# Performance work log

Measured on AMD Instinct MI355X. Metric: run time of the kernel, lower is better.

Reference implementation:

```python
import jax, jax.numpy as jnp
import numpy as np
from jax import lax


def _conv(x, w, padding, groups=1):
    # NCHW / OIHW 2D conv, stride 1
    return lax.conv_general_dilated(
        x, w, window_strides=(1, 1), padding=padding,
        dimension_numbers=("NCHW", "OIHW", "NCHW"),
        feature_group_count=groups)


def setup_inputs() -> dict:
    key = jax.random.key(0)
    ks = jax.random.split(key, 5)
    B, C, H, W = 8, 192, 128, 128
    HEADS = 8
    rgb = jax.random.normal(ks[0], (B, C, H, W), dtype=jnp.float32)
    ir = jax.random.normal(ks[1], (B, C, H, W), dtype=jnp.float32)
    w_qkv = jax.random.normal(ks[2], (3 * C, C, 1, 1), dtype=jnp.float32) * 0.02
    w_dw = jax.random.normal(ks[3], (3 * C, 1, 3, 3), dtype=jnp.float32) * 0.02
    w_proj = jax.random.normal(ks[4], (C, C, 1, 1), dtype=jnp.float32) * 0.02
    temperature = jnp.ones((HEADS, 1, 1), dtype=jnp.float32)
    return {"rgb": rgb, "ir": ir, "w_qkv": w_qkv, "w_dw": w_dw,
            "w_proj": w_proj, "temperature": temperature}


def reference(rgb, ir, w_qkv, w_dw, w_proj, temperature):
    heads = temperature.shape[0]
    b, c, h, w = rgb.shape
    hd = c // heads  # per-head channel count

    def qkv(x):
        y = _conv(x, w_qkv, "VALID")                 # [b, 3c, h, w]
        y = _conv(y, w_dw, "SAME", groups=3 * c)      # depthwise 3x3
        q, k, v = jnp.split(y, 3, axis=1)
        rs = lambda t: t.reshape(b, heads, hd, h * w)  # b head c (h w)
        return rs(q), rs(k), rs(v)

    rq, rk, rv = qkv(rgb)
    iq, ik, iv = qkv(ir)

    # torch F.normalize(dim=-1): x / max(||x||_2, 1e-12)
    nrm = lambda t: t / jnp.maximum(jnp.linalg.norm(t, axis=-1, keepdims=True), 1e-12)
    rq, rk, iq, ik = nrm(rq), nrm(rk), nrm(iq), nrm(ik)

    # channel-wise (transposed) cross attention: [b,h,hd,hd] attn matrices
    attn_ir = jax.nn.softmax(jnp.einsum("bhcn,bhdn->bhcd", rq, ik) * temperature, axis=-1)
    attn_rgb = jax.nn.softmax(jnp.einsum("bhcn,bhdn->bhcd", iq, rk) * temperature, axis=-1)

    out_ir = jnp.einsum("bhcd,bhdn->bhcn", attn_ir, iv).reshape(b, c, h, w)
    out_rgb = jnp.einsum("bhcd,bhdn->bhcn", attn_rgb, rv).reshape(b, c, h, w)

    out_ir = _conv(out_ir, w_proj, "VALID")
    out_rgb = _conv(out_rgb, w_proj, "VALID")
    return out_rgb, out_ir
```

## Files before the change

### kernel.cpp

```cpp
#include <hip/hip_runtime.h>

#define N_PIX 16384
#define CC    192
#define C3    576
#define KK    192
#define HD    24

typedef __attribute__((ext_vector_type(8))) short short8;
typedef __attribute__((ext_vector_type(4))) float f32x4;

__device__ __forceinline__ unsigned short f2bf(float x) {
    unsigned u = __float_as_uint(x);
    u += 0x7fff + ((u >> 16) & 1);
    return (unsigned short)(u >> 16);
}
__device__ __forceinline__ float bf2f(unsigned short s) {
    return __uint_as_float(((unsigned)s) << 16);
}
__device__ __forceinline__ int pack2(unsigned short lo, unsigned short hi) {
    return (int)(((unsigned)hi << 16) | (unsigned)lo);
}

__global__ __launch_bounds__(256) void cvt_f32_bf16(const float* __restrict__ src,
                                                    unsigned short* __restrict__ dst, int n4) {
    int i = blockIdx.x * 256 + threadIdx.x;
    if (i < n4) {
        float4 v = ((const float4*)src)[i];
        ushort4 o;
        o.x = f2bf(v.x); o.y = f2bf(v.y); o.z = f2bf(v.z); o.w = f2bf(v.w);
        ((ushort4*)dst)[i] = o;
    }
}

template<bool B_F32, bool C_BF16>
__device__ __forceinline__ void mfma_gemm(const unsigned short* __restrict__ Abf,
                                          const void* __restrict__ Bsrc,
                                          void* __restrict__ Cdst,
                                          int m0, int n0) {
    __shared__ unsigned short As[192][44];
    __shared__ unsigned short Bs[128][44];

    const int tid  = threadIdx.x;
    const int wave = tid >> 6, lane = tid & 63;
    const int quad = lane >> 4, l15 = lane & 15;
    const int wr = wave >> 2, wc = wave & 3;

    f32x4 acc[6][2];
#pragma unroll
    for (int i = 0; i < 6; i++)
#pragma unroll
        for (int j = 0; j < 2; j++) acc[i][j] = (f32x4)0.f;

    const int kg = tid & 7;
    const int n2 = tid >> 3;

    for (int k0 = 0; k0 < KK; k0 += 32) {
        {
            int row = tid >> 2, kc = (tid & 3) * 8;
            *(int4*)&As[row][kc] = *(const int4*)(Abf + (long)(m0 + row) * KK + k0 + kc);
            if (tid < 256) {
                int ch = tid + 512;
                int row2 = ch >> 2, kc2 = (ch & 3) * 8;
                *(int4*)&As[row2][kc2] = *(const int4*)(Abf + (long)(m0 + row2) * KK + k0 + kc2);
            }
        }
        if (B_F32) {
            const float* Bp = (const float*)Bsrc;
            float2 v[4];
#pragma unroll
            for (int j = 0; j < 4; j++)
                v[j] = *(const float2*)(Bp + (long)(k0 + kg * 4 + j) * N_PIX + n0 + n2 * 2);
#pragma unroll
            for (int i = 0; i < 2; i++) {
                unsigned short us[4];
#pragma unroll
                for (int j = 0; j < 4; j++) us[j] = f2bf(i ? v[j].y : v[j].x);
                int2 pk = make_int2(pack2(us[0], us[1]), pack2(us[2], us[3]));
                *(int2*)&Bs[n2 * 2 + i][kg * 4] = pk;
            }
        } else {
            const unsigned short* Bp = (const unsigned short*)Bsrc;
            ushort2 v[4];
#pragma unroll
            for (int j = 0; j < 4; j++)
                v[j] = *(const ushort2*)(Bp + (long)(k0 + kg * 4 + j) * N_PIX + n0 + n2 * 2);
#pragma unroll
            for (int i = 0; i < 2; i++) {
                unsigned short us[4];
#pragma unroll
                for (int j = 0; j < 4; j++) us[j] = i ? v[j].y : v[j].x;
                int2 pk = make_int2(pack2(us[0], us[1]), pack2(us[2], us[3]));
                *(int2*)&Bs[n2 * 2 + i][kg * 4] = pk;
            }
        }
        __syncthreads();

        short8 a[6], b[2];
#pragma unroll
        for (int mi = 0; mi < 6; mi++)
            a[mi] = *(const short8*)&As[wr * 96 + mi * 16 + l15][quad * 8];
#pragma unroll
        for (int ni = 0; ni < 2; ni++)
            b[ni] = *(const short8*)&Bs[wc * 32 + ni * 16 + l15][quad * 8];
#pragma unroll
        for (int mi = 0; mi < 6; mi++)
#pragma unroll
            for (int ni = 0; ni < 2; ni++)
                acc[mi][ni] = __builtin_amdgcn_mfma_f32_16x16x32_bf16(a[mi], b[ni], acc[mi][ni], 0, 0, 0);
        __syncthreads();
    }

#pragma unroll
    for (int mi = 0; mi < 6; mi++)
#pragma unroll
        for (int ni = 0; ni < 2; ni++)
#pragma unroll
            for (int r = 0; r < 4; r++) {
                int row = m0 + wr * 96 + mi * 16 + quad * 4 + r;
                int col = n0 + wc * 32 + ni * 16 + l15;
                if (C_BF16)
                    ((unsigned short*)Cdst)[(long)row * N_PIX + col] = f2bf(acc[mi][ni][r]);
                else
                    ((float*)Cdst)[(long)row * N_PIX + col] = acc[mi][ni][r];
            }
}

__global__ __launch_bounds__(512, 4) void qkv_mfma(const unsigned short* __restrict__ wbf,
                                                   const float* __restrict__ rgb,
                                                   const float* __restrict__ ir,
                                                   unsigned short* __restrict__ Ybf) {
    const int z = blockIdx.z, mod = z >> 3, b = z & 7;
    const float* x = (mod ? ir : rgb) + (long)b * CC * N_PIX;
    unsigned short* y = Ybf + (long)z * C3 * N_PIX;
    mfma_gemm<true, true>(wbf, x, y, blockIdx.y * 192, blockIdx.x * 128);
}

__global__ __launch_bounds__(512, 4) void out_mfma(const unsigned short* __restrict__ weff,
                                                   const unsigned short* __restrict__ Zbf,
                                                   float* __restrict__ out) {
    const int z = blockIdx.z;
    const unsigned short* V = Zbf + ((long)z * C3 + 2 * CC) * N_PIX;
    float* C = out + (long)z * CC * N_PIX;
    mfma_gemm<false, false>(weff + (long)z * CC * CC, V, C, 0, blockIdx.x * 128);
}

__global__ __launch_bounds__(256) void dwconv3x3(const unsigned short* __restrict__ Ybf,
                                                 const float* __restrict__ wdw,
                                                 unsigned short* __restrict__ Zbf) {
    const int z  = blockIdx.z;
    const int oc = blockIdx.y;
    const int idx = blockIdx.x * 256 + threadIdx.x;
    const int p0  = idx * 8;
    const int h   = p0 >> 7;
    const int w0  = p0 & 127;
    const int wq  = threadIdx.x & 15;
    const unsigned short* Yc = Ybf + ((long)z * C3 + oc) * N_PIX;

    float wk[9];
#pragma unroll
    for (int i = 0; i < 9; i++) wk[i] = wdw[oc * 9 + i];

    float f[3][8];
#pragma unroll
    for (int ry = 0; ry < 3; ry++) {
        const int hy = h + ry - 1;
        int4 raw = make_int4(0, 0, 0, 0);
        if (hy >= 0 && hy <= 127)
            raw = *(const int4*)(Yc + hy * 128 + w0);
        f[ry][0] = bf2f((unsigned short)(raw.x & 0xffff));
        f[ry][1] = bf2f((unsigned short)((unsigned)raw.x >> 16));
        f[ry][2] = bf2f((unsigned short)(raw.y & 0xffff));
        f[ry][3] = bf2f((unsigned short)((unsigned)raw.y >> 16));
        f[ry][4] = bf2f((unsigned short)(raw.z & 0xffff));
        f[ry][5] = bf2f((unsigned short)((unsigned)raw.z >> 16));
        f[ry][6] = bf2f((unsigned short)(raw.w & 0xffff));
        f[ry][7] = bf2f((unsigned short)((unsigned)raw.w >> 16));
    }

    float acc[8];
#pragma unroll
    for (int j = 0; j < 8; j++) acc[j] = 0.f;

#pragma unroll
    for (int ry = 0; ry < 3; ry++) {
        float l = __shfl_up(f[ry][7], 1);
        float r = __shfl_down(f[ry][0], 1);
        if (wq == 0)  l = 0.f;
        if (wq == 15) r = 0.f;
        const float wl = wk[ry * 3 + 0], wc = wk[ry * 3 + 1], wr = wk[ry * 3 + 2];
        acc[0] = fmaf(wl, l, acc[0]);
#pragma unroll
        for (int j = 1; j < 8; j++) acc[j] = fmaf(wl, f[ry][j - 1], acc[j]);
#pragma unroll
        for (int j = 0; j < 8; j++) acc[j] = fmaf(wc, f[ry][j], acc[j]);
#pragma unroll
        for (int j = 0; j < 7; j++) acc[j] = fmaf(wr, f[ry][j + 1], acc[j]);
        acc[7] = fmaf(wr, r, acc[7]);
    }

    ushort4 o[2];
    unsigned short* po = (unsigned short*)o;
#pragma unroll
    for (int j = 0; j < 8; j++) po[j] = f2bf(acc[j]);
    *(int4*)(Zbf + ((long)z * C3 + oc) * N_PIX + p0) = *(const int4*)o;
}

__global__ __launch_bounds__(64) void gram_partial(const unsigned short* __restrict__ Zbf,
                                                   float* __restrict__ gpart) {
    const int split = blockIdx.x;
    const int bh    = blockIdx.y;
    const int which = blockIdx.z;
    const int b = bh >> 3, head = bh & 7;
    const int zq = (which == 0) ? b : 8 + b;
    const int zk = (which == 0) ? 8 + b : b;
    const unsigned short* Q  = Zbf + ((long)zq * C3 + head * HD) * N_PIX;
    const unsigned short* Kr = Zbf + ((long)zk * C3 + CC + head * HD) * N_PIX;

    __shared__ float Qc[24][132];
    __shared__ float Kc[24][132];

    const int t = threadIdx.x;
    const int ci = t >> 3, di = t & 7;
    const int c0 = ci * 3, d0 = di * 3;

    float acc[3][3];
#pragma unroll
    for (int i = 0; i < 3; i++)
#pragma unroll
        for (int j = 0; j < 3; j++) acc[i][j] = 0.f;
    float ss = 0.f;

    const int n0base = split * 2048;
    for (int nc = 0; nc < 2048; nc += 128) {
        const long n0 = n0base + nc;
        const unsigned short* src = nullptr;
        float* dstrow = nullptr;
        if (t < 24)               { src = Q  + (long)t * N_PIX + n0;        dstrow = Qc[t]; }
        else if (t >= 32 && t < 56) { src = Kr + (long)(t - 32) * N_PIX + n0; dstrow = Kc[t - 32]; }
        if (src) {
#pragma unroll 4
            for (int i = 0; i < 16; i++) {
                int4 raw = *(const int4*)(src + i * 8);
                float f[8];
                f[0] = bf2f((unsigned short)(raw.x & 0xffff)); f[1] = bf2f((unsigned short)((unsigned)raw.x >> 16));
                f[2] = bf2f((unsigned short)(raw.y & 0xffff)); f[3] = bf2f((unsigned short)((unsigned)raw.y >> 16));
                f[4] = bf2f((unsigned short)(raw.z & 0xffff)); f[5] = bf2f((unsigned short)((unsigned)raw.z >> 16));
                f[6] = bf2f((unsigned short)(raw.w & 0xffff)); f[7] = bf2f((unsigned short)((unsigned)raw.w >> 16));
                *(float4*)&dstrow[i * 8]     = make_float4(f[0], f[1], f[2], f[3]);
                *(float4*)&dstrow[i * 8 + 4] = make_float4(f[4], f[5], f[6], f[7]);
#pragma unroll
                for (int q = 0; q < 8; q++) ss = fmaf(f[q], f[q], ss);
            }
        }
        __syncthreads();
#pragma unroll 4
        for (int kk = 0; kk < 128; kk += 4) {
            float4 qv[3], kv[3];
#pragma unroll
            for (int i = 0; i < 3; i++) qv[i] = *(const float4*)&Qc[c0 + i][kk];
#pragma unroll
            for (int j = 0; j < 3; j++) kv[j] = *(const float4*)&Kc[d0 + j][kk];
#pragma unroll
            for (int i = 0; i < 3; i++)
#pragma unroll
                for (int j = 0; j < 3; j++)
                    acc[i][j] += qv[i].x * kv[j].x + qv[i].y * kv[j].y +
                                 qv[i].z * kv[j].z + qv[i].w * kv[j].w;
        }
        __syncthreads();
    }

    const int g = (which * 64 + bh) * 8 + split;
    float* gp = gpart + (long)g * 624;
#pragma unroll
    for (int i = 0; i < 3; i++)
#pragma unroll
        for (int j = 0; j < 3; j++)
            gp[(c0 + i) * 24 + (d0 + j)] = acc[i][j];
    if (t < 24) gp[576 + t] = ss;
    else if (t >= 32 && t < 56) gp[600 + (t - 32)] = ss;
}

__global__ __launch_bounds__(256) void gram_reduce_softmax(const float* __restrict__ gpart,
                                                           const float* __restrict__ temperature,
                                                           float* __restrict__ P) {
    const int g = blockIdx.x;
    const int head = g & 7;
    __shared__ float Gs[576];
    __shared__ float qs[24], ks[24], invq[24], invk[24];

    const int t = threadIdx.x;
    for (int e = t; e < 624; e += 256) {
        float s = 0.f;
        for (int sp = 0; sp < 8; sp++) s += gpart[(long)(g * 8 + sp) * 624 + e];
        if (e < 576) Gs[e] = s;
        else if (e < 600) qs[e - 576] = s;
        else ks[e - 600] = s;
    }
    __syncthreads();
    if (t < 24) {
        invq[t] = 1.f / fmaxf(sqrtf(qs[t]), 1e-12f);
        invk[t] = 1.f / fmaxf(sqrtf(ks[t]), 1e-12f);
    }
    __syncthreads();
    if (t < 24) {
        const float temp = temperature[head];
        float row[24];
        float m = -1e30f;
#pragma unroll
        for (int d = 0; d < 24; d++) {
            row[d] = Gs[t * 24 + d] * invq[t] * invk[d] * temp;
            m = fmaxf(m, row[d]);
        }
        float ssum = 0.f;
#pragma unroll
        for (int d = 0; d < 24; d++) {
            row[d] = expf(row[d] - m);
            ssum += row[d];
        }
        const float inv = 1.f / ssum;
#pragma unroll
        for (int d = 0; d < 24; d++)
            P[(long)g * 576 + t * 24 + d] = row[d] * inv;
    }
}

__global__ __launch_bounds__(256) void build_weff(const float* __restrict__ wproj,
                                                  const float* __restrict__ P,
                                                  unsigned short* __restrict__ weff) {
    const int o = blockIdx.z, b = blockIdx.y;
    const int e = blockIdx.x * 256 + threadIdx.x;
    const int co = e / 192, col = e % 192;
    const int head = col / 24, d = col % 24;
    const int which = 1 - o;
    const float* Pp = P + (long)(which * 64 + b * 8 + head) * 576;
    const float* wp = wproj + co * 192 + head * 24;
    float acc = 0.f;
#pragma unroll
    for (int hc = 0; hc < 24; hc++)
        acc = fmaf(wp[hc], Pp[hc * 24 + d], acc);
    weff[((long)(o * 8 + b) * 192 + co) * 192 + col] = f2bf(acc);
}

extern "C" void kernel_launch(void* const* d_in, const int* in_sizes, int n_in,
                              void* d_out, int out_size, void* d_ws, size_t ws_size,
                              hipStream_t stream) {
    (void)in_sizes; (void)n_in; (void)out_size; (void)ws_size;
    const float* rgb    = (const float*)d_in[0];
    const float* ir     = (const float*)d_in[1];
    const float* w_qkv  = (const float*)d_in[2];
    const float* w_dw   = (const float*)d_in[3];
    const float* w_proj = (const float*)d_in[4];
    const float* temp   = (const float*)d_in[5];
    float* out = (float*)d_out;

    char* wsb = (char*)d_ws;
    unsigned short* Y_bf    = (unsigned short*)(wsb);
    unsigned short* Z_bf    = (unsigned short*)(wsb + 301989888L);
    unsigned short* w_bf    = (unsigned short*)(wsb + 603979776L);
    unsigned short* weff_bf = (unsigned short*)(wsb + 604200960L);
    float*          gpart   = (float*)(wsb + 605380608L);
    float*          P       = (float*)(wsb + 607936512L);

    cvt_f32_bf16<<<108, 256, 0, stream>>>(w_qkv, w_bf, 27648);
    qkv_mfma<<<dim3(128, 3, 16), 512, 0, stream>>>(w_bf, rgb, ir, Y_bf);
    dwconv3x3<<<dim3(8, 576, 16), 256, 0, stream>>>(Y_bf, w_dw, Z_bf);
    gram_partial<<<dim3(8, 64, 2), 64, 0, stream>>>(Z_bf, gpart);
    gram_reduce_softmax<<<128, 256, 0, stream>>>(gpart, temp, P);
    build_weff<<<dim3(144, 8, 2), 256, 0, stream>>>(w_proj, P, weff_bf);
    out_mfma<<<dim3(128, 1, 16), 512, 0, stream>>>(weff_bf, Z_bf, out);
}
```

Before: 807.5 us.

## Pre-transpose inputs to bf16 and pipeline QKV GEMM with direct global-to-LDS loads

Adds a kernel that converts the fp32 rgb/ir inputs to bf16 and transposes them to pixel-major layout, so the QKV GEMM can stream contiguous K-rows. The QKV GEMM is rewritten to use global_load_lds 16-byte transfers into XOR-swizzled, double-buffered shared memory with a K-step of 64. This removes per-thread fp32 to bf16 conversion and strided loads from the GEMM's inner loop. The cost is an extra pass over the inputs, and the Z buffer is reused as scratch for the transposed data.

```diff
diff --git a/kernel.cpp b/kernel.cpp
--- a/kernel.cpp
+++ b/kernel.cpp
@@ -5,6 +5,7 @@
 #define C3    576
 #define KK    192
 #define HD    24
+#define KS    64
 
 typedef __attribute__((ext_vector_type(8))) short short8;
 typedef __attribute__((ext_vector_type(4))) float f32x4;
@@ -19,6 +20,12 @@
 }
 __device__ __forceinline__ int pack2(unsigned short lo, unsigned short hi) {
     return (int)(((unsigned)hi << 16) | (unsigned)lo);
+}
+
+__device__ __forceinline__ void g2l16(const unsigned short* g, unsigned short* l) {
+    __builtin_amdgcn_global_load_lds(
+        (const __attribute__((address_space(1))) void*)g,
+        (__attribute__((address_space(3))) void*)l, 16, 0, 0);
 }
 
 __global__ __launch_bounds__(256) void cvt_f32_bf16(const float* __restrict__ src,
@@ -32,11 +39,126 @@
     }
 }
 
-template<bool B_F32, bool C_BF16>
-__device__ __forceinline__ void mfma_gemm(const unsigned short* __restrict__ Abf,
-                                          const void* __restrict__ Bsrc,
-                                          void* __restrict__ Cdst,
-                                          int m0, int n0) {
+__global__ __launch_bounds__(256) void cvtT(const float* __restrict__ rgb,
+                                            const float* __restrict__ ir,
+                                            unsigned short* __restrict__ xT) {
+    const int z  = blockIdx.y;
+    const int n0 = blockIdx.x * 128;
+    const float* x = ((z >= 8) ? ir : rgb) + (long)(z & 7) * CC * N_PIX;
+    __shared__ unsigned short T[192][136];
+
+    const int t = threadIdx.x;
+#pragma unroll
+    for (int i = 0; i < 24; i++) {
+        int q = i * 256 + t;
+        int k = q >> 5, nc = q & 31;
+        float4 v = *(const float4*)(x + (long)k * N_PIX + n0 + nc * 4);
+        ushort4 o;
+        o.x = f2bf(v.x); o.y = f2bf(v.y); o.z = f2bf(v.z); o.w = f2bf(v.w);
+        *(ushort4*)&T[k][nc * 4] = o;
+    }
+    __syncthreads();
+    unsigned short* dst = xT + ((long)z * N_PIX + n0) * CC;
+#pragma unroll
+    for (int i = 0; i < 12; i++) {
+        int c = i * 256 + t;
+        int n = c / 24, kc = c - n * 24;
+        unsigned short us[8];
+#pragma unroll
+        for (int j = 0; j < 8; j++) us[j] = T[kc * 8 + j][n];
+        int4 pk = make_int4(pack2(us[0], us[1]), pack2(us[2], us[3]),
+                            pack2(us[4], us[5]), pack2(us[6], us[7]));
+        *(int4*)(dst + (long)n * CC + kc * 8) = pk;
+    }
+}
+
+__global__ __launch_bounds__(512, 4) void qkv_mfma(const unsigned short* __restrict__ wbf,
+                                                   const unsigned short* __restrict__ xT,
+                                                   unsigned short* __restrict__ Ybf) {
+    const int z  = blockIdx.z;
+    const unsigned short* Bg = xT + (long)z * N_PIX * CC;
+    unsigned short* y = Ybf + (long)z * C3 * N_PIX;
+    const int m0 = blockIdx.y * 192, n0 = blockIdx.x * 128;
+
+    __shared__ unsigned short As[2][192 * 64];
+    __shared__ unsigned short Bs[2][128 * 64];
+
+    const int tid  = threadIdx.x;
+    const int wave = tid >> 6, lane = tid & 63;
+    const int quad = lane >> 4, l15 = lane & 15;
+    const int wr = wave >> 2, wc = wave & 3;
+
+    f32x4 acc[6][2];
+#pragma unroll
+    for (int i = 0; i < 6; i++)
+#pragma unroll
+        for (int j = 0; j < 2; j++) acc[i][j] = (f32x4)0.f;
+
+    auto stage = [&](int buf, int k0) {
+#pragma unroll
+        for (int s = 0; s < 3; s++) {
+            int j = s * 8 + wave;
+            int q = j * 64 + lane;
+            int m = q >> 3, c = (q & 7) ^ (m & 7);
+            g2l16(wbf + (long)(m0 + m) * KK + k0 + c * 8, &As[buf][j * 512]);
+        }
+#pragma unroll
+        for (int s = 0; s < 2; s++) {
+            int j = s * 8 + wave;
+            int q = j * 64 + lane;
+            int n = q >> 3, c = (q & 7) ^ (n & 7);
+            g2l16(Bg + (long)(n0 + n) * CC + k0 + c * 8, &Bs[buf][j * 512]);
+        }
+    };
+
+    stage(0, 0);
+    __syncthreads();
+    int cur = 0;
+    for (int it = 0; it < 3; ++it) {
+        if (it < 2) stage(cur ^ 1, (it + 1) * KS);
+        const unsigned short* A  = As[cur];
+        const unsigned short* Bl = Bs[cur];
+#pragma unroll
+        for (int kk = 0; kk < 2; kk++) {
+            short8 a[6], b[2];
+#pragma unroll
+            for (int mi = 0; mi < 6; mi++) {
+                int r = wr * 96 + mi * 16 + l15;
+                int c = (kk * 4 + quad) ^ (r & 7);
+                a[mi] = *(const short8*)&A[r * 64 + c * 8];
+            }
+#pragma unroll
+            for (int ni = 0; ni < 2; ni++) {
+                int n = wc * 32 + ni * 16 + l15;
+                int c = (kk * 4 + quad) ^ (n & 7);
+                b[ni] = *(const short8*)&Bl[n * 64 + c * 8];
+            }
+#pragma unroll
+            for (int mi = 0; mi < 6; mi++)
+#pragma unroll
+                for (int ni = 0; ni < 2; ni++)
+                    acc[mi][ni] = __builtin_amdgcn_mfma_f32_16x16x32_bf16(a[mi], b[ni], acc[mi][ni], 0, 0, 0);
+        }
+        __syncthreads();
+        cur ^= 1;
+    }
+
+#pragma unroll
+    for (int mi = 0; mi < 6; mi++)
+#pragma unroll
+        for (int ni = 0; ni < 2; ni++)
+#pragma unroll
+            for (int r = 0; r < 4; r++) {
+                int row = m0 + wr * 96 + mi * 16 + quad * 4 + r;
+                int col = n0 + wc * 32 + ni * 16 + l15;
+                y[(long)row * N_PIX + col] = f2bf(acc[mi][ni][r]);
+            }
+}
+
+__device__ __forceinline__ void mfma_gemm_old(const unsigned short* __restrict__ Abf,
+                                              const unsigned short* __restrict__ Bsrc,
+                                              float* __restrict__ Cdst,
+                                              int m0, int n0) {
     __shared__ unsigned short As[192][44];
     __shared__ unsigned short Bs[128][44];
 
@@ -64,26 +186,11 @@
                 *(int4*)&As[row2][kc2] = *(const int4*)(Abf + (long)(m0 + row2) * KK + k0 + kc2);
             }
         }
-        if (B_F32) {
-            const float* Bp = (const float*)Bsrc;
-            float2 v[4];
+        {
+            ushort2 v[4];
 #pragma unroll
             for (int j = 0; j < 4; j++)
-                v[j] = *(const float2*)(Bp + (long)(k0 + kg * 4 + j) * N_PIX + n0 + n2 * 2);
-#pragma unroll
-            for (int i = 0; i < 2; i++) {
-                unsigned short us[4];
-#pragma unroll
-                for (int j = 0; j < 4; j++) us[j] = f2bf(i ? v[j].y : v[j].x);
-                int2 pk = make_int2(pack2(us[0], us[1]), pack2(us[2], us[3]));
-                *(int2*)&Bs[n2 * 2 + i][kg * 4] = pk;
-            }
-        } else {
-            const unsigned short* Bp = (const unsigned short*)Bsrc;
-            ushort2 v[4];
-#pragma unroll
-            for (int j = 0; j < 4; j++)
-                v[j] = *(const ushort2*)(Bp + (long)(k0 + kg * 4 + j) * N_PIX + n0 + n2 * 2);
+                v[j] = *(const ushort2*)(Bsrc + (long)(k0 + kg * 4 + j) * N_PIX + n0 + n2 * 2);
 #pragma unroll
             for (int i = 0; i < 2; i++) {
                 unsigned short us[4];
@@ -118,21 +225,8 @@
             for (int r = 0; r < 4; r++) {
                 int row = m0 + wr * 96 + mi * 16 + quad * 4 + r;
                 int col = n0 + wc * 32 + ni * 16 + l15;
-                if (C_BF16)
-                    ((unsigned short*)Cdst)[(long)row * N_PIX + col] = f2bf(acc[mi][ni][r]);
-                else
-                    ((float*)Cdst)[(long)row * N_PIX + col] = acc[mi][ni][r];
-            }
-}
-
-__global__ __launch_bounds__(512, 4) void qkv_mfma(const unsigned short* __restrict__ wbf,
-                                                   const float* __restrict__ rgb,
-                                                   const float* __restrict__ ir,
-                                                   unsigned short* __restrict__ Ybf) {
-    const int z = blockIdx.z, mod = z >> 3, b = z & 7;
-    const float* x = (mod ? ir : rgb) + (long)b * CC * N_PIX;
-    unsigned short* y = Ybf + (long)z * C3 * N_PIX;
-    mfma_gemm<true, true>(wbf, x, y, blockIdx.y * 192, blockIdx.x * 128);
+                Cdst[(long)row * N_PIX + col] = acc[mi][ni][r];
+            }
 }
 
 __global__ __launch_bounds__(512, 4) void out_mfma(const unsigned short* __restrict__ weff,
@@ -141,7 +235,7 @@
     const int z = blockIdx.z;
     const unsigned short* V = Zbf + ((long)z * C3 + 2 * CC) * N_PIX;
     float* C = out + (long)z * CC * N_PIX;
-    mfma_gemm<false, false>(weff + (long)z * CC * CC, V, C, 0, blockIdx.x * 128);
+    mfma_gemm_old(weff + (long)z * CC * CC, V, C, 0, blockIdx.x * 128);
 }
 
 __global__ __launch_bounds__(256) void dwconv3x3(const unsigned short* __restrict__ Ybf,
@@ -357,13 +451,15 @@
     char* wsb = (char*)d_ws;
     unsigned short* Y_bf    = (unsigned short*)(wsb);
     unsigned short* Z_bf    = (unsigned short*)(wsb + 301989888L);
+    unsigned short* xT_bf   = Z_bf;
     unsigned short* w_bf    = (unsigned short*)(wsb + 603979776L);
     unsigned short* weff_bf = (unsigned short*)(wsb + 604200960L);
     float*          gpart   = (float*)(wsb + 605380608L);
     float*          P       = (float*)(wsb + 607936512L);
 
     cvt_f32_bf16<<<108, 256, 0, stream>>>(w_qkv, w_bf, 27648);
-    qkv_mfma<<<dim3(128, 3, 16), 512, 0, stream>>>(w_bf, rgb, ir, Y_bf);
+    cvtT<<<dim3(128, 16), 256, 0, stream>>>(rgb, ir, xT_bf);
+    qkv_mfma<<<dim3(128, 3, 16), 512, 0, stream>>>(w_bf, xT_bf, Y_bf);
     dwconv3x3<<<dim3(8, 576, 16), 256, 0, stream>>>(Y_bf, w_dw, Z_bf);
     gram_partial<<<dim3(8, 64, 2), 64, 0, stream>>>(Z_bf, gpart);
     gram_reduce_softmax<<<128, 256, 0, stream>>>(gpart, temp, P);
```

Result: no change. 799.4 us (-1.0%).
